# Performance work log

Measured on AMD Instinct MI355X. Metric: run time of the kernel, lower is better.

Reference implementation:

```python
import jax, jax.numpy as jnp
import numpy as np
import math

B, S, E, A, H, L, V = 2, 2048, 512, 512, 8, 4, 50257
HD = A // H  # 64 per-head dim (attention_size // n_heads)
PAD = 0
EPS = 1e-5

def _sin_pe():
    pos = np.arange(S)[:, None].astype(np.float32)
    div = np.exp(np.arange(0, E, 2).astype(np.float32) * (-math.log(10000.0) / E))
    pe = np.zeros((S, E), dtype=np.float32)
    pe[:, 0::2] = np.sin(pos * div)
    pe[:, 1::2] = np.cos(pos * div)
    return jnp.asarray(pe)

PE = _sin_pe()

def setup_inputs():
    key = jax.random.key(0)
    ks = jax.random.split(key, 20)
    s = 0.02
    emb = jax.random.normal(ks[0], (V, E), jnp.float32) * s
    emb = emb.at[PAD].set(0.0)  # nn.Embedding padding_idx row is zero
    return {
        "input_ids": jax.random.randint(ks[1], (B, S), 0, V, dtype=jnp.int32),
        "attention_mask": jnp.ones((B, S), jnp.int32),
        "emb": emb,
        "Wq": jax.random.normal(ks[2], (L, H, E, HD), jnp.float32) * s,
        "Wk": jax.random.normal(ks[3], (L, H, E, HD), jnp.float32) * s,
        "Wv": jax.random.normal(ks[4], (L, H, E, HD), jnp.float32) * s,
        "Wo": jax.random.normal(ks[5], (L, A, E), jnp.float32) * s,
        "ln1_g": jnp.ones((L, E), jnp.float32),
        "ln1_b": jnp.zeros((L, E), jnp.float32),
        "ln2_g": jnp.ones((L, E), jnp.float32),
        "ln2_b": jnp.zeros((L, E), jnp.float32),
        "ff_w1": jax.random.normal(ks[6], (L, E, 4 * E), jnp.float32) * s,
        "ff_b1": jnp.zeros((L, 4 * E), jnp.float32),
        "ff_w2": jax.random.normal(ks[7], (L, 4 * E, E), jnp.float32) * s,
        "ff_b2": jnp.zeros((L, E), jnp.float32),
        "lnf_g": jnp.ones((E,), jnp.float32),
        "lnf_b": jnp.zeros((E,), jnp.float32),
        "Wout": jax.random.normal(ks[8], (E, V), jnp.float32) * s,
        "bout": jnp.zeros((V,), jnp.float32),
    }

def _ln(x, g, b):
    m = jnp.mean(x, axis=-1, keepdims=True)
    v = jnp.mean((x - m) ** 2, axis=-1, keepdims=True)
    return (x - m) / jnp.sqrt(v + EPS) * g + b

def reference(input_ids, attention_mask, emb, Wq, Wk, Wv, Wo, ln1_g, ln1_b, ln2_g, ln2_b, ff_w1, ff_b1, ff_w2, ff_b2, lnf_g, lnf_b, Wout, bout):
    # mask: padding (attention_mask==0) broadcast over queries, OR causal upper triangle
    pad = (attention_mask == 0)[:, None, :]                  # [B,1,S]
    causal = jnp.triu(jnp.ones((S, S), bool), 1)             # [S,S]
    mask = (pad | causal)[:, None, :, :]                     # [B,1,S,S]
    x = emb[input_ids] + PE[None, :S]                        # [B,S,E]
    scale = 1.0 / math.sqrt(HD)

    def block(x, p):
        wq, wk, wv, wo, g1, b1, g2, b2, w1, c1, w2, c2 = p
        xn = _ln(x, g1, b1)
        q = jnp.einsum('bse,hed->bhsd', xn, wq)
        k = jnp.einsum('bse,hed->bhsd', xn, wk)
        v = jnp.einsum('bse,hed->bhsd', xn, wv)
        scores = jnp.einsum('bhsd,bhtd->bhst', q, k) * scale  # masked_fill(-inf) then /sqrt(dk) == mask after scale
        scores = jnp.where(mask, -jnp.inf, scores)
        p_attn = jax.nn.softmax(scores, axis=-1)
        attn = jnp.einsum('bhst,bhtd->bhsd', p_attn, v)
        attn = attn.transpose(0, 2, 1, 3).reshape(B, S, A)    # concat heads
        x = x + attn @ wo                                     # residual + out proj (no bias)
        xn2 = _ln(x, g2, b2)
        h = jax.nn.gelu(xn2 @ w1 + c1, approximate=False)     # nn.GELU default (erf)
        x = x + h @ w2 + c2
        return x, None

    params = (Wq, Wk, Wv, Wo, ln1_g, ln1_b, ln2_g, ln2_b, ff_w1, ff_b1, ff_w2, ff_b2)
    x, _ = jax.lax.scan(block, x, params)
    return _ln(x, lnf_g, lnf_b) @ Wout + bout                 # [B,S,V]
```

## Files before the change

kernel.cpp:

```cpp
#include <hip/hip_runtime.h>
#include <math.h>

#define BB 2
#define SS 2048
#define EE 512
#define HH 8
#define HD 64
#define LL 4
#define VV 50257
#define NTOK (BB*SS)
#define VPAD2 50432

typedef __bf16 bf16_t;
typedef bf16_t bf16x8 __attribute__((ext_vector_type(8)));
typedef float  f32x4  __attribute__((ext_vector_type(4)));

__device__ __forceinline__ void gload_lds16(const void* g, void* l) {
  __builtin_amdgcn_global_load_lds(
      (const __attribute__((address_space(1))) void*)g,
      (__attribute__((address_space(3))) void*)l, 16, 0, 0);
}

__global__ __launch_bounds__(256) void embed_kernel(const int* __restrict__ ids,
                                                    const float* __restrict__ emb,
                                                    float* __restrict__ x) {
  int idx = blockIdx.x * 256 + threadIdx.x;
  int e   = idx & (EE - 1);
  int tok = idx >> 9;
  int s   = tok & (SS - 1);
  int id  = ids[tok];
  float freq = expf((float)(e & ~1) * -0.01798894604f);
  float ang  = (float)s * freq;
  float pe   = (e & 1) ? cosf(ang) : sinf(ang);
  x[idx] = emb[(size_t)id * EE + e] + pe;
}

__global__ __launch_bounds__(256) void ln_kernel(const float* __restrict__ in,
                                                 bf16_t* __restrict__ out,
                                                 const float* __restrict__ g,
                                                 const float* __restrict__ b) {
  int wv = threadIdx.x >> 6, lane = threadIdx.x & 63;
  int row = blockIdx.x * 4 + wv;
  const float4* r = reinterpret_cast<const float4*>(in + (size_t)row * EE) + lane * 2;
  float4 v0 = r[0], v1 = r[1];
  float s = v0.x + v0.y + v0.z + v0.w + v1.x + v1.y + v1.z + v1.w;
#pragma unroll
  for (int o = 32; o > 0; o >>= 1) s += __shfl_xor(s, o);
  float mean = s * (1.f / EE);
  float d0 = v0.x-mean, d1 = v0.y-mean, d2 = v0.z-mean, d3 = v0.w-mean;
  float d4 = v1.x-mean, d5 = v1.y-mean, d6 = v1.z-mean, d7 = v1.w-mean;
  float var = d0*d0+d1*d1+d2*d2+d3*d3+d4*d4+d5*d5+d6*d6+d7*d7;
#pragma unroll
  for (int o = 32; o > 0; o >>= 1) var += __shfl_xor(var, o);
  float inv = rsqrtf(var * (1.f / EE) + 1e-5f);
  const float4* gp = reinterpret_cast<const float4*>(g) + lane * 2;
  const float4* bp = reinterpret_cast<const float4*>(b) + lane * 2;
  float4 g0 = gp[0], g1 = gp[1], b0 = bp[0], b1 = bp[1];
  bf16_t tmp[8];
  tmp[0] = (bf16_t)(d0*inv*g0.x + b0.x); tmp[1] = (bf16_t)(d1*inv*g0.y + b0.y);
  tmp[2] = (bf16_t)(d2*inv*g0.z + b0.z); tmp[3] = (bf16_t)(d3*inv*g0.w + b0.w);
  tmp[4] = (bf16_t)(d4*inv*g1.x + b1.x); tmp[5] = (bf16_t)(d5*inv*g1.y + b1.y);
  tmp[6] = (bf16_t)(d6*inv*g1.z + b1.z); tmp[7] = (bf16_t)(d7*inv*g1.w + b1.w);
  *reinterpret_cast<bf16x8*>(out + (size_t)row * EE + lane * 8) = *reinterpret_cast<bf16x8*>(tmp);
}

__device__ __forceinline__ void transpose_tile(const float* __restrict__ ip,
                                               bf16_t* __restrict__ op,
                                               int k0, int n0, int ldin, int ldout,
                                               int Nvalid, float* T) {
  int t = threadIdx.x;
  int r = t >> 2, cb = (t & 3) * 16;
#pragma unroll
  for (int i = 0; i < 16; i++) {
    int n = n0 + cb + i;
    T[r * 65 + cb + i] = (n < Nvalid) ? ip[(size_t)(k0 + r) * ldin + n] : 0.f;
  }
  __syncthreads();
  bf16_t tmp[16];
#pragma unroll
  for (int i = 0; i < 16; i++) tmp[i] = (bf16_t)T[(cb + i) * 65 + r];
  bf16_t* o = op + (size_t)(n0 + r) * ldout + k0 + cb;
  *reinterpret_cast<bf16x8*>(o)     = *reinterpret_cast<bf16x8*>(&tmp[0]);
  *reinterpret_cast<bf16x8*>(o + 8) = *reinterpret_cast<bf16x8*>(&tmp[8]);
}

__global__ __launch_bounds__(256) void wconv_kernel(const float* __restrict__ in,
                                                    bf16_t* __restrict__ out,
                                                    int ldin, int ldout, int Nvalid,
                                                    long zin, long zout) {
  __shared__ float T[64 * 65];
  transpose_tile(in + (size_t)blockIdx.z * zin, out + (size_t)blockIdx.z * zout,
                 blockIdx.x * 64, blockIdx.y * 64, ldin, ldout, Nvalid, T);
}

__global__ __launch_bounds__(256) void wconv_qkv_kernel(const float* __restrict__ Wq,
                                                        const float* __restrict__ Wk,
                                                        const float* __restrict__ Wv,
                                                        bf16_t* __restrict__ out) {
  __shared__ float T[64 * 65];
  int z = blockIdx.z;
  int l = z / 24, rem = z % 24, sec = rem >> 3, h = rem & 7;
  const float* W = sec == 0 ? Wq : (sec == 1 ? Wk : Wv);
  const float* ip = W + (size_t)(l * 8 + h) * (EE * HD);
  bf16_t* op = out + (size_t)l * (1536 * 512) + (size_t)(sec * 512 + h * 64) * 512;
  transpose_tile(ip, op, blockIdx.x * 64, 0, HD, EE, HD, T);
}

template<int MODE, int TM>
__global__ __launch_bounds__(256) void gemm_bf16(
    const bf16_t* __restrict__ A, const bf16_t* __restrict__ Bt,
    int M, int N, int K,
    const float* __restrict__ bias,
    float* __restrict__ Cf, bf16_t* __restrict__ Cb,
    bf16_t* __restrict__ qo, bf16_t* __restrict__ ko, bf16_t* __restrict__ vo) {
  constexpr int MI = TM / 32;
  __shared__ __align__(16) bf16_t As[TM * 64];
  __shared__ __align__(16) bf16_t Bs[128 * 64];
  int tid = threadIdx.x, lane = tid & 63, w = tid >> 6;
  int lr = lane & 15, lg = lane >> 4;
  int m0 = blockIdx.y * TM, n0 = blockIdx.x * 128;
  f32x4 acc[MI][4];
#pragma unroll
  for (int i = 0; i < MI; i++)
#pragma unroll
    for (int j = 0; j < 4; j++) acc[i][j] = (f32x4){0.f, 0.f, 0.f, 0.f};
  int wr = w >> 1, wc = w & 1;

  const bf16_t* Abase = A  + (size_t)(m0 + lr) * K + lg * 8;
  const bf16_t* Bbase = Bt + (size_t)(n0 + lr) * K + lg * 8;

  for (int k0 = 0; k0 < K; k0 += 64) {
#pragma unroll
    for (int i = 0; i < MI; i++) {
      int c = w * MI + i;
      gload_lds16(Abase + (size_t)(c >> 1) * 16 * K + k0 + (c & 1) * 32,
                  (char*)As + c * 1024);
    }
#pragma unroll
    for (int i = 0; i < 4; i++) {
      int c = w * 4 + i;
      gload_lds16(Bbase + (size_t)(c >> 1) * 16 * K + k0 + (c & 1) * 32,
                  (char*)Bs + c * 1024);
    }
    __syncthreads();
#pragma unroll
    for (int kk = 0; kk < 2; kk++) {
      bf16x8 afr[MI], bfr[4];
#pragma unroll
      for (int mi = 0; mi < MI; mi++)
        afr[mi] = *reinterpret_cast<const bf16x8*>(
            &As[(((wr * MI + mi) << 1) + kk) * 512 + lane * 8]);
#pragma unroll
      for (int ni = 0; ni < 4; ni++)
        bfr[ni] = *reinterpret_cast<const bf16x8*>(
            &Bs[(((wc * 4 + ni) << 1) + kk) * 512 + lane * 8]);
#pragma unroll
      for (int mi = 0; mi < MI; mi++)
#pragma unroll
        for (int ni = 0; ni < 4; ni++)
          acc[mi][ni] = __builtin_amdgcn_mfma_f32_16x16x32_bf16(afr[mi], bfr[ni], acc[mi][ni], 0, 0, 0);
    }
    __syncthreads();
  }

#pragma unroll
  for (int mi = 0; mi < MI; mi++)
#pragma unroll
    for (int ni = 0; ni < 4; ni++) {
      int colg = n0 + wc * 64 + ni * 16 + lr;
#pragma unroll
      for (int j = 0; j < 4; j++) {
        int rowg = m0 + wr * (TM / 2) + mi * 16 + lg * 4 + j;
        float v = acc[mi][ni][j];
        if (MODE == 0) {
          int sec = colg >> 9, cc = colg & 511, hh = cc >> 6, dd = cc & 63;
          int bi = rowg >> 11, s = rowg & 2047;
          if (sec == 0)      qo[(((size_t)bi * HH + hh) * SS + s) * HD + dd] = (bf16_t)(v * 0.125f);
          else if (sec == 1) ko[(((size_t)bi * HH + hh) * SS + s) * HD + dd] = (bf16_t)v;
          else               vo[(((size_t)bi * HH + hh) * HD + dd) * SS + s] = (bf16_t)v;
        } else if (MODE == 1) {
          v += bias[colg];
          v = 0.5f * v * (1.f + erff(v * 0.70710678f));
          Cb[(size_t)rowg * N + colg] = (bf16_t)v;
        } else {
          if (bias) v += bias[colg];
          Cf[(size_t)rowg * EE + colg] += v;
        }
      }
    }
}

__global__ __launch_bounds__(512) void gemm256_out(
    const bf16_t* __restrict__ A, const bf16_t* __restrict__ Bt,
    const float* __restrict__ bias, float* __restrict__ C) {
  __shared__ __align__(16) bf16_t As[256 * 64];
  __shared__ __align__(16) bf16_t Bs[256 * 64];
  int tid = threadIdx.x, lane = tid & 63, w = tid >> 6;
  int lr = lane & 15, lg = lane >> 4;
  int bid = blockIdx.x;
  int n0 = (bid % 197) * 256, m0 = (bid / 197) * 256;
  int wr = w >> 2, wc = w & 3;
  f32x4 acc[8][4];
#pragma unroll
  for (int i = 0; i < 8; i++)
#pragma unroll
    for (int j = 0; j < 4; j++) acc[i][j] = (f32x4){0.f, 0.f, 0.f, 0.f};

  const bf16_t* Abase = A  + (size_t)(m0 + lr) * 512 + lg * 8;
  const bf16_t* Bbase = Bt + (size_t)(n0 + lr) * 512 + lg * 8;

  for (int k0 = 0; k0 < 512; k0 += 64) {
#pragma unroll
    for (int i = 0; i < 4; i++) {
      int c = w * 4 + i;
      gload_lds16(Abase + (size_t)(c >> 1) * 16 * 512 + k0 + (c & 1) * 32,
                  (char*)As + c * 1024);
      gload_lds16(Bbase + (size_t)(c >> 1) * 16 * 512 + k0 + (c & 1) * 32,
                  (char*)Bs + c * 1024);
    }
    __syncthreads();
#pragma unroll
    for (int kk = 0; kk < 2; kk++) {
      bf16x8 afr[8], bfr[4];
#pragma unroll
      for (int mi = 0; mi < 8; mi++)
        afr[mi] = *reinterpret_cast<const bf16x8*>(
            &As[(((wr * 8 + mi) << 1) + kk) * 512 + lane * 8]);
#pragma unroll
      for (int ni = 0; ni < 4; ni++)
        bfr[ni] = *reinterpret_cast<const bf16x8*>(
            &Bs[(((wc * 4 + ni) << 1) + kk) * 512 + lane * 8]);
#pragma unroll
      for (int mi = 0; mi < 8; mi++)
#pragma unroll
        for (int ni = 0; ni < 4; ni++)
          acc[mi][ni] = __builtin_amdgcn_mfma_f32_16x16x32_bf16(afr[mi], bfr[ni], acc[mi][ni], 0, 0, 0);
    }
    __syncthreads();
  }

#pragma unroll
  for (int mi = 0; mi < 8; mi++)
#pragma unroll
    for (int ni = 0; ni < 4; ni++) {
      int colg = n0 + wc * 64 + ni * 16 + lr;
      if (colg < VV) {
        float bs = bias[colg];
#pragma unroll
        for (int j = 0; j < 4; j++) {
          int rowg = m0 + wr * 128 + mi * 16 + lg * 4 + j;
          C[(size_t)rowg * VV + colg] = acc[mi][ni][j] + bs;
        }
      }
    }
}

#define QBLK 64
#define KVB 64
__global__ __launch_bounds__(256) void attn_kernel(
    const bf16_t* __restrict__ qb,
    const bf16_t* __restrict__ kb,
    const bf16_t* __restrict__ vT,
    const int* __restrict__ amask,
    bf16_t* __restrict__ ab) {
  __shared__ bf16_t Qs[QBLK][72];
  __shared__ bf16_t Ps[QBLK][72];
  __shared__ __align__(16) bf16_t Ks[2][KVB * 64];
  __shared__ __align__(16) bf16_t Vs[2][KVB * 64];
  __shared__ float kmAll[SS];
  int tid = threadIdx.x, lane = tid & 63, w = tid >> 6;
  int lr = lane & 15, lg = lane >> 4;
  int bid = blockIdx.x;
  int bh = bid & 15;
  int qi = bid >> 4;
  int qq = (qi < 16) ? qi : 47 - qi;
  int q0 = qq * QBLK;
  int b = bh >> 3, h = bh & 7;
  const bf16_t* Qg = qb + (size_t)bh * SS * HD;
  const bf16_t* Kg = kb + (size_t)bh * SS * HD;
  const bf16_t* Vg = vT + (size_t)bh * HD * SS;

  {
    int r = tid >> 2, c = (tid & 3) * 16;
    const uint4* s = reinterpret_cast<const uint4*>(Qg + (size_t)(q0 + r) * HD + c);
    uint4 a0 = s[0], a1 = s[1];
    *reinterpret_cast<uint4*>(&Qs[r][c])     = a0;
    *reinterpret_cast<uint4*>(&Qs[r][c + 8]) = a1;
  }
#pragma unroll
  for (int i = 0; i < 8; i++) {
    int s = i * 256 + tid;
    kmAll[s] = amask[b * SS + s] ? 0.f : -1e30f;
  }

  auto stageKV = [&](int buf, int kv0) {
#pragma unroll
    for (int i = 0; i < 4; i++) {
      int c = w * 4 + i;
      if (c < 8) {
        gload_lds16(Kg + (size_t)(kv0 + (c >> 1) * 16 + lr) * HD + (c & 1) * 32 + lg * 8,
                    (char*)&Ks[buf][0] + c * 1024);
      } else {
        int cc = c - 8;
        gload_lds16(Vg + (size_t)((cc >> 1) * 16 + lr) * SS + kv0 + (cc & 1) * 32 + lg * 8,
                    (char*)&Vs[buf][0] + cc * 1024);
      }
    }
  };

  f32x4 o[4];
  f32x4 m_run, l_run;
  m_run = (f32x4){-1e30f, -1e30f, -1e30f, -1e30f};
  l_run = (f32x4){0.f, 0.f, 0.f, 0.f};
#pragma unroll
  for (int nd = 0; nd < 4; nd++) o[nd] = (f32x4){0.f, 0.f, 0.f, 0.f};

  stageKV(0, 0);
  __syncthreads();

  int ntile = qq + 1;
  for (int t = 0; t < ntile; t++) {
    int buf = t & 1;
    int kv0 = t * KVB;
    if (t + 1 < ntile) stageKV(buf ^ 1, kv0 + KVB);

    f32x4 sc[4];
#pragma unroll
    for (int ni = 0; ni < 4; ni++) sc[ni] = (f32x4){0.f, 0.f, 0.f, 0.f};
#pragma unroll
    for (int kk = 0; kk < 2; kk++) {
      bf16x8 af = *reinterpret_cast<const bf16x8*>(&Qs[w * 16 + lr][kk * 32 + lg * 8]);
      bf16x8 bf[4];
#pragma unroll
      for (int ni = 0; ni < 4; ni++)
        bf[ni] = *reinterpret_cast<const bf16x8*>(&Ks[buf][((ni << 1) + kk) * 512 + lane * 8]);
#pragma unroll
      for (int ni = 0; ni < 4; ni++)
        sc[ni] = __builtin_amdgcn_mfma_f32_16x16x32_bf16(af, bf[ni], sc[ni], 0, 0, 0);
    }

    {
      int qrb = q0 + w * 16 + lg * 4;
      float kmv[4];
#pragma unroll
      for (int ni = 0; ni < 4; ni++) kmv[ni] = kmAll[kv0 + ni * 16 + lr];
#pragma unroll
      for (int ni = 0; ni < 4; ni++) {
        int kg = kv0 + ni * 16 + lr;
#pragma unroll
        for (int j = 0; j < 4; j++) {
          float s = sc[ni][j] + kmv[ni];
          sc[ni][j] = (kg <= qrb + j) ? s : -1e30f;
        }
      }
      f32x4 rmax = sc[0];
#pragma unroll
      for (int ni = 1; ni < 4; ni++)
#pragma unroll
        for (int j = 0; j < 4; j++) rmax[j] = fmaxf(rmax[j], sc[ni][j]);
#pragma unroll
      for (int msk = 1; msk <= 8; msk <<= 1)
#pragma unroll
        for (int j = 0; j < 4; j++) rmax[j] = fmaxf(rmax[j], __shfl_xor(rmax[j], msk));
      f32x4 mnew, corr;
#pragma unroll
      for (int j = 0; j < 4; j++) {
        mnew[j] = fmaxf(m_run[j], rmax[j]);
        corr[j] = __expf(m_run[j] - mnew[j]);
      }
      m_run = mnew;
      f32x4 rs = (f32x4){0.f, 0.f, 0.f, 0.f};
#pragma unroll
      for (int ni = 0; ni < 4; ni++) {
#pragma unroll
        for (int j = 0; j < 4; j++) {
          float p = __expf(sc[ni][j] - mnew[j]);
          rs[j] += p;
          Ps[w * 16 + lg * 4 + j][ni * 16 + lr] = (bf16_t)p;
        }
      }
#pragma unroll
      for (int msk = 1; msk <= 8; msk <<= 1)
#pragma unroll
        for (int j = 0; j < 4; j++) rs[j] += __shfl_xor(rs[j], msk);
#pragma unroll
      for (int j = 0; j < 4; j++) l_run[j] = l_run[j] * corr[j] + rs[j];
#pragma unroll
      for (int nd = 0; nd < 4; nd++) o[nd] = o[nd] * corr;
    }

#pragma unroll
    for (int kc = 0; kc < 2; kc++) {
      bf16x8 pa = *reinterpret_cast<const bf16x8*>(&Ps[w * 16 + lr][kc * 32 + lg * 8]);
      bf16x8 vb[4];
#pragma unroll
      for (int nd = 0; nd < 4; nd++)
        vb[nd] = *reinterpret_cast<const bf16x8*>(&Vs[buf][((nd << 1) + kc) * 512 + lane * 8]);
#pragma unroll
      for (int nd = 0; nd < 4; nd++)
        o[nd] = __builtin_amdgcn_mfma_f32_16x16x32_bf16(pa, vb[nd], o[nd], 0, 0, 0);
    }
    asm volatile("s_waitcnt vmcnt(0)" ::: "memory");
    asm volatile("s_barrier" ::: "memory");
  }

  f32x4 linv;
#pragma unroll
  for (int j = 0; j < 4; j++) linv[j] = 1.f / l_run[j];
#pragma unroll
  for (int nd = 0; nd < 4; nd++)
#pragma unroll
    for (int j = 0; j < 4; j++) {
      int rowg = b * SS + q0 + w * 16 + lg * 4 + j;
      int col = h * HD + nd * 16 + lr;
      ab[(size_t)rowg * EE + col] = (bf16_t)(o[nd][j] * linv[j]);
    }
}

extern "C" void kernel_launch(void* const* d_in, const int* in_sizes, int n_in,
                              void* d_out, int out_size, void* d_ws, size_t ws_size,
                              hipStream_t stream) {
  const int*   ids   = (const int*)d_in[0];
  const int*   amask = (const int*)d_in[1];
  const float* emb   = (const float*)d_in[2];
  const float* Wq    = (const float*)d_in[3];
  const float* Wk    = (const float*)d_in[4];
  const float* Wv    = (const float*)d_in[5];
  const float* Wo    = (const float*)d_in[6];
  const float* ln1g  = (const float*)d_in[7];
  const float* ln1b  = (const float*)d_in[8];
  const float* ln2g  = (const float*)d_in[9];
  const float* ln2b  = (const float*)d_in[10];
  const float* fw1   = (const float*)d_in[11];
  const float* fb1   = (const float*)d_in[12];
  const float* fw2   = (const float*)d_in[13];
  const float* fb2   = (const float*)d_in[14];
  const float* lnfg  = (const float*)d_in[15];
  const float* lnfb  = (const float*)d_in[16];
  const float* Wout  = (const float*)d_in[17];
  const float* bout  = (const float*)d_in[18];
  float* out = (float*)d_out;

  float*  x     = (float*)d_ws;
  bf16_t* xn    = (bf16_t*)((char*)d_ws + (8u << 20));
  bf16_t* WoutT = (bf16_t*)((char*)d_ws + (12u << 20));
  char* sc = (char*)d_out;
  bf16_t* qbuf = (bf16_t*)(sc);
  bf16_t* kbuf = (bf16_t*)(sc + 4194304);
  bf16_t* vTb  = (bf16_t*)(sc + 8388608);
  bf16_t* ab   = (bf16_t*)(sc + 12582912);
  bf16_t* hb   = (bf16_t*)(sc + 16777216);
  bf16_t* Wqkv = (bf16_t*)(sc + 33554432);
  bf16_t* WoT  = (bf16_t*)(sc + 39845888);
  bf16_t* W1T  = (bf16_t*)(sc + 41943040);
  bf16_t* W2T  = (bf16_t*)(sc + 50331648);

  wconv_qkv_kernel<<<dim3(8, 1, 96), 256, 0, stream>>>(Wq, Wk, Wv, Wqkv);
  wconv_kernel<<<dim3(8, 8, LL), 256, 0, stream>>>(Wo, WoT, 512, 512, 512,
                                                   512L * 512, 512L * 512);
  wconv_kernel<<<dim3(8, 32, LL), 256, 0, stream>>>(fw1, W1T, 2048, 512, 2048,
                                                    512L * 2048, 2048L * 512);
  wconv_kernel<<<dim3(32, 8, LL), 256, 0, stream>>>(fw2, W2T, 512, 2048, 512,
                                                    2048L * 512, 512L * 2048);
  wconv_kernel<<<dim3(8, VPAD2 / 64, 1), 256, 0, stream>>>(Wout, WoutT, VV, 512, VV, 0, 0);

  embed_kernel<<<NTOK * EE / 256, 256, 0, stream>>>(ids, emb, x);

  for (int l = 0; l < LL; l++) {
    ln_kernel<<<NTOK / 4, 256, 0, stream>>>(x, xn, ln1g + l * EE, ln1b + l * EE);
    gemm_bf16<0, 128><<<dim3(12, 32), 256, 0, stream>>>(xn, Wqkv + (size_t)l * 1536 * 512,
        NTOK, 1536, 512, nullptr, nullptr, nullptr, qbuf, kbuf, vTb);
    attn_kernel<<<dim3(512), 256, 0, stream>>>(qbuf, kbuf, vTb, amask, ab);
    gemm_bf16<2, 64><<<dim3(4, 64), 256, 0, stream>>>(ab, WoT + (size_t)l * 512 * 512,
        NTOK, 512, 512, nullptr, x, nullptr, nullptr, nullptr, nullptr);
    ln_kernel<<<NTOK / 4, 256, 0, stream>>>(x, xn, ln2g + l * EE, ln2b + l * EE);
    gemm_bf16<1, 128><<<dim3(16, 32), 256, 0, stream>>>(xn, W1T + (size_t)l * 2048 * 512,
        NTOK, 2048, 512, fb1 + l * 2048, nullptr, hb, nullptr, nullptr, nullptr);
    gemm_bf16<2, 64><<<dim3(4, 64), 256, 0, stream>>>(hb, W2T + (size_t)l * 512 * 2048,
        NTOK, 512, 2048, fb2 + l * EE, x, nullptr, nullptr, nullptr, nullptr);
  }
  ln_kernel<<<NTOK / 4, 256, 0, stream>>>(x, xn, lnfg, lnfb);
  gemm256_out<<<dim3(16 * (VPAD2 / 256)), 512, 0, stream>>>(xn, WoutT, bout, out);
}
```

Measured before the change: 1.375 ms.

## Double-buffer GEMM LDS tiles with async global-to-LDS prefetch

The bf16 MFMA GEMM kernel now keeps two LDS buffers for its A and B tiles. It issues the global_load_lds for the next K tile before computing on the current one, using explicit vmcnt waits and raw s_barrier in place of __syncthreads. The aim is to overlap global memory latency with MFMA work across K iterations. This doubles LDS use, which may lower occupancy, and its correctness depends on the exact vmcnt count (MI+4 outstanding loads) and on LDS writes having landed before the barrier.

```diff
diff --git a/kernel.cpp b/kernel.cpp
--- a/kernel.cpp
+++ b/kernel.cpp
@@ -114,8 +114,9 @@
     float* __restrict__ Cf, bf16_t* __restrict__ Cb,
     bf16_t* __restrict__ qo, bf16_t* __restrict__ ko, bf16_t* __restrict__ vo) {
   constexpr int MI = TM / 32;
-  __shared__ __align__(16) bf16_t As[TM * 64];
-  __shared__ __align__(16) bf16_t Bs[128 * 64];
+  constexpr int LW = MI + 4;
+  __shared__ __align__(16) bf16_t As[2][TM * 64];
+  __shared__ __align__(16) bf16_t Bs[2][128 * 64];
   int tid = threadIdx.x, lane = tid & 63, w = tid >> 6;
   int lr = lane & 15, lg = lane >> 4;
   int m0 = blockIdx.y * TM, n0 = blockIdx.x * 128;
@@ -129,38 +130,50 @@
   const bf16_t* Abase = A  + (size_t)(m0 + lr) * K + lg * 8;
   const bf16_t* Bbase = Bt + (size_t)(n0 + lr) * K + lg * 8;
 
-  for (int k0 = 0; k0 < K; k0 += 64) {
+  auto stage = [&](int buf, int k0) {
 #pragma unroll
     for (int i = 0; i < MI; i++) {
       int c = w * MI + i;
       gload_lds16(Abase + (size_t)(c >> 1) * 16 * K + k0 + (c & 1) * 32,
-                  (char*)As + c * 1024);
+                  (char*)&As[buf][0] + c * 1024);
     }
 #pragma unroll
     for (int i = 0; i < 4; i++) {
       int c = w * 4 + i;
       gload_lds16(Bbase + (size_t)(c >> 1) * 16 * K + k0 + (c & 1) * 32,
-                  (char*)Bs + c * 1024);
-    }
-    __syncthreads();
+                  (char*)&Bs[buf][0] + c * 1024);
+    }
+  };
+
+  int nk = K >> 6;
+  stage(0, 0);
+  for (int k = 0; k < nk; k++) {
+    int cur = k & 1;
+    if (k + 1 < nk) {
+      stage(cur ^ 1, (k + 1) << 6);
+      asm volatile("s_waitcnt vmcnt(%0)" :: "i"(LW) : "memory");
+    } else {
+      asm volatile("s_waitcnt vmcnt(0)" ::: "memory");
+    }
+    __builtin_amdgcn_s_barrier();
 #pragma unroll
     for (int kk = 0; kk < 2; kk++) {
       bf16x8 afr[MI], bfr[4];
 #pragma unroll
       for (int mi = 0; mi < MI; mi++)
         afr[mi] = *reinterpret_cast<const bf16x8*>(
-            &As[(((wr * MI + mi) << 1) + kk) * 512 + lane * 8]);
+            &As[cur][(((wr * MI + mi) << 1) + kk) * 512 + lane * 8]);
 #pragma unroll
       for (int ni = 0; ni < 4; ni++)
         bfr[ni] = *reinterpret_cast<const bf16x8*>(
-            &Bs[(((wc * 4 + ni) << 1) + kk) * 512 + lane * 8]);
+            &Bs[cur][(((wc * 4 + ni) << 1) + kk) * 512 + lane * 8]);
 #pragma unroll
       for (int mi = 0; mi < MI; mi++)
 #pragma unroll
         for (int ni = 0; ni < 4; ni++)
           acc[mi][ni] = __builtin_amdgcn_mfma_f32_16x16x32_bf16(afr[mi], bfr[ni], acc[mi][ni], 0, 0, 0);
     }
-    __syncthreads();
+    __builtin_amdgcn_s_barrier();
   }
 
 #pragma unroll
```

After: 1.363 ms. About the same (-0.9%).
